# Kernel optimization log

Measured on AMD Instinct MI355X. Metric: run time of the kernel, lower is better.

The kernel has to match this reference:

```python
import jax, jax.numpy as jnp
import numpy as np

N, CIN, COUT, T, V, K = 32, 256, 256, 128, 25, 3
BN_EPS = 1e-5


def setup_inputs() -> dict:
    key = jax.random.key(0)
    k0, k1, k2 = jax.random.split(key, 3)
    x = jax.random.normal(k0, (N, CIN, T, V), dtype=jnp.float32)
    A = jax.random.normal(k1, (K, V, V), dtype=jnp.float32)
    W = jax.random.normal(k2, (K * COUT, CIN), dtype=jnp.float32) * 0.02
    b = jnp.zeros((K * COUT,), dtype=jnp.float32)
    gamma = jnp.ones((COUT,), dtype=jnp.float32)
    beta = jnp.zeros((COUT,), dtype=jnp.float32)
    return {"x": x, "A": A, "W": W, "b": b, "gamma": gamma, "beta": beta}


def reference(x, A, W, b, gamma, beta):
    n, c, t, v = x.shape
    k = A.shape[0]
    # 1x1 conv (conv_pos='pre'): [n,c,t,v] x [k*cout, c] -> [n, k*cout, t, v]
    y = jnp.einsum('nctv,oc->notv', x, W) + b[None, :, None, None]
    # split subsets and contract joints against the k adjacency matrices
    y = y.reshape(n, k, -1, t, v)
    y = jnp.einsum('nkctv,kvw->nctw', y, A)
    # BatchNorm2d (training-mode batch stats over n,t,v per channel)
    mu = jnp.mean(y, axis=(0, 2, 3), keepdims=True)
    var = jnp.var(y, axis=(0, 2, 3), keepdims=True)
    yn = (y - mu) * jax.lax.rsqrt(var + BN_EPS)
    out = gamma[None, :, None, None] * yn + beta[None, :, None, None]
    # with_res=False -> residual is 0; ReLU activation
    return jax.nn.relu(out)
```

## Files before the change

### kernel.cpp

```cpp
#include <hip/hip_runtime.h>
#include <cstddef>

#define NN   32
#define CIN  256
#define COUT 256
#define TT   128
#define VV   25
#define KK   3
#define TV   (TT*VV)
#define NTVC (NN*TT*VV)
#define BN_EPS 1e-5f

#define YT_LD 104
#define XS_LD 264

typedef __attribute__((ext_vector_type(8))) short bf16x8;
typedef __attribute__((ext_vector_type(4))) float f32x4;

__device__ __forceinline__ unsigned short f2bf(float f) {
    unsigned int u = __float_as_uint(f);
    u = (u + 0x7fffu + ((u >> 16) & 1u)) >> 16;
    return (unsigned short)u;
}

__device__ __forceinline__ uint2 pk4(f32x4 v) {
    uint2 r;
    asm("v_cvt_pk_bf16_f32 %0, %1, %2" : "=v"(r.x) : "v"(v[0]), "v"(v[1]));
    asm("v_cvt_pk_bf16_f32 %0, %1, %2" : "=v"(r.y) : "v"(v[2]), "v"(v[3]));
    return r;
}

__global__ __launch_bounds__(256)
void convert_w_kernel(const float* __restrict__ W, unsigned short* __restrict__ Wb) {
    int i = blockIdx.x * 256 + threadIdx.x;
    Wb[i] = f2bf(W[i]);
}

__global__ __launch_bounds__(256)
void transpose_x_kernel(const float* __restrict__ x, unsigned short* __restrict__ xT) {
    __shared__ float T[64][65];
    const int n   = blockIdx.z;
    const int s0  = blockIdx.x * 64;
    const int c0  = blockIdx.y * 64;
    const int tid = threadIdx.x;
    const int r    = tid >> 4;
    const int col4 = (tid & 15) * 4;

    const float* xp = x + (size_t)(n * CIN + c0) * TV + s0;
    for (int rr = r; rr < 64; rr += 16) {
        float4 v = *(const float4*)(xp + (size_t)rr * TV + col4);
        T[rr][col4 + 0] = v.x; T[rr][col4 + 1] = v.y;
        T[rr][col4 + 2] = v.z; T[rr][col4 + 3] = v.w;
    }
    __syncthreads();
    unsigned short* op = xT + ((size_t)n * TV + s0) * CIN + c0;
    for (int ss = r; ss < 64; ss += 16) {
        ushort4 o;
        o.x = f2bf(T[col4 + 0][ss]);
        o.y = f2bf(T[col4 + 1][ss]);
        o.z = f2bf(T[col4 + 2][ss]);
        o.w = f2bf(T[col4 + 3][ss]);
        *(ushort4*)(op + (size_t)ss * CIN + col4) = o;
    }
}

__global__ __launch_bounds__(1024)
void gemm_adj_kernel(const unsigned short* __restrict__ xT,
                     const unsigned short* __restrict__ Wb,
                     const float* __restrict__ A,
                     const float* __restrict__ b,
                     float* __restrict__ y2,
                     float* __restrict__ statsN)
{
    __shared__ __align__(16) unsigned short U[CIN * YT_LD];
    __shared__ __align__(16) unsigned short Ab[32 * 96];

    const int tid  = threadIdx.x;
    const int lane = tid & 63;
    const int wg   = tid >> 6;
    const int ln15 = lane & 15;
    const int quad = lane >> 4;
    const int tp   = blockIdx.x & 63;
    const int n    = blockIdx.x >> 6;
    const int t0   = tp * 2;

    {
        const unsigned short* xsrc = xT + ((size_t)n * TV + (size_t)t0 * VV) * CIN;
        for (int ch = tid; ch < 1600; ch += 1024) {
            const int s = ch >> 5, c8 = ch & 31;
            *(bf16x8*)&U[s * XS_LD + c8 * 8] = *(const bf16x8*)&xsrc[ch * 8];
        }
        const bf16x8 z = {0,0,0,0,0,0,0,0};
        for (int ch = tid; ch < 231; ch += 1024) {
            const int rr = 50 + ch / 33, c8 = ch - (ch / 33) * 33;
            *(bf16x8*)&U[rr * XS_LD + c8 * 8] = z;
        }
        for (int i = tid; i < 32 * 96; i += 1024) {
            const int w = i / 96, kv = i - w * 96;
            const int k = kv >> 5, v = kv & 31;
            Ab[i] = f2bf((v < VV && w < VV) ? A[k * VV * VV + v * VV + w] : 0.f);
        }
    }

    f32x4 acc[4][3];
    #pragma unroll
    for (int nt = 0; nt < 3; ++nt) {
        const float bv = b[48 * wg + 16 * nt + ln15];
        #pragma unroll
        for (int mt = 0; mt < 4; ++mt)
            #pragma unroll
            for (int r = 0; r < 4; ++r)
                acc[mt][nt][r] = bv;
    }

    __syncthreads();

    const int soff[4] = {0, 16, 25, 41};
    const unsigned short* wp = Wb + (size_t)(48 * wg + ln15) * CIN + quad * 8;
    bf16x8 wbuf[2][3];
    #pragma unroll
    for (int nt = 0; nt < 3; ++nt)
        wbuf[0][nt] = *(const bf16x8*)(wp + (size_t)nt * 16 * CIN);

    #pragma unroll
    for (int ks = 0; ks < 8; ++ks) {
        const int cur = ks & 1, nxt = cur ^ 1;
        if (ks < 7) {
            #pragma unroll
            for (int nt = 0; nt < 3; ++nt)
                wbuf[nxt][nt] = *(const bf16x8*)(wp + (size_t)nt * 16 * CIN + (ks + 1) * 32);
        }
        bf16x8 xfr[4];
        #pragma unroll
        for (int mt = 0; mt < 4; ++mt)
            xfr[mt] = *(const bf16x8*)&U[(soff[mt] + ln15) * XS_LD + ks * 32 + quad * 8];
        #pragma unroll
        for (int mt = 0; mt < 4; ++mt)
            #pragma unroll
            for (int nt = 0; nt < 3; ++nt)
                acc[mt][nt] = __builtin_amdgcn_mfma_f32_16x16x32_bf16(
                                  xfr[mt], wbuf[cur][nt], acc[mt][nt], 0, 0, 0);
    }

    __syncthreads();

    for (int i = tid; i < CIN * 21; i += 1024) {
        const int c = i / 21, rr = i - c * 21;
        const int k = rr / 7, v = VV + (rr - k * 7);
        U[c * YT_LD + k * 32 + v] = 0;
    }

    const int obase = 48 * wg + ln15;

    auto write_half = [&](int h) {
        const int mtF = 2 * h, mtP = 2 * h + 1;
        {
            const int v0 = quad * 4;
            #pragma unroll
            for (int nt = 0; nt < 3; ++nt) {
                const int o = obase + 16 * nt;
                *(uint2*)&U[(o & 255) * YT_LD + (o >> 8) * 32 + v0] = pk4(acc[mtF][nt]);
            }
        }
        if (quad < 2) {
            const int v0 = 16 + quad * 4;
            #pragma unroll
            for (int nt = 0; nt < 3; ++nt) {
                const int o = obase + 16 * nt;
                *(uint2*)&U[(o & 255) * YT_LD + (o >> 8) * 32 + v0] = pk4(acc[mtP][nt]);
            }
        } else if (quad == 2) {
            #pragma unroll
            for (int nt = 0; nt < 3; ++nt) {
                const int o = obase + 16 * nt;
                U[(o & 255) * YT_LD + (o >> 8) * 32 + 24] = f2bf(acc[mtP][nt][0]);
            }
        }
    };

    bf16x8 bq[3][2];
    float bsum1[4], bsum2[4];
    #pragma unroll
    for (int r = 0; r < 4; ++r) { bsum1[r] = 0.f; bsum2[r] = 0.f; }
    const int cb = wg * 16;

    #pragma unroll
    for (int h = 0; h < 2; ++h) {
        if (h) __syncthreads();
        write_half(h);
        __syncthreads();

        if (h == 0) {
            #pragma unroll
            for (int k = 0; k < 3; ++k)
                #pragma unroll
                for (int nw = 0; nw < 2; ++nw)
                    bq[k][nw] = *(const bf16x8*)&Ab[(16 * nw + ln15) * 96 + k * 32 + quad * 8];
        }

        f32x4 a2[2];
        #pragma unroll
        for (int nw = 0; nw < 2; ++nw)
            #pragma unroll
            for (int r = 0; r < 4; ++r) a2[nw][r] = 0.f;
        #pragma unroll
        for (int k = 0; k < 3; ++k) {
            const bf16x8 af = *(const bf16x8*)&U[(cb + ln15) * YT_LD + k * 32 + quad * 8];
            a2[0] = __builtin_amdgcn_mfma_f32_16x16x32_bf16(af, bq[k][0], a2[0], 0, 0, 0);
            a2[1] = __builtin_amdgcn_mfma_f32_16x16x32_bf16(af, bq[k][1], a2[1], 0, 0, 0);
        }
        const int t = t0 + h;
        float* op = y2 + (size_t)n * COUT * TV
                       + (size_t)(cb + 4 * quad) * TV + (size_t)t * VV;
        #pragma unroll
        for (int r = 0; r < 4; ++r) {
            const float va = a2[0][r];
            const float vb = a2[1][r];
            op[r * TV + ln15] = va;
            if (ln15 < 9) op[r * TV + 16 + ln15] = vb;
            const float vbm = (ln15 < 9) ? vb : 0.f;
            bsum1[r] += va + vbm;
            bsum2[r] += va * va + vbm * vbm;
        }
    }

    #pragma unroll
    for (int r = 0; r < 4; ++r) {
        float s1 = bsum1[r], s2 = bsum2[r];
        #pragma unroll
        for (int off = 1; off < 16; off <<= 1) {
            s1 += __shfl_xor(s1, off);
            s2 += __shfl_xor(s2, off);
        }
        if (ln15 == 0) {
            const int c = cb + 4 * quad + r;
            atomicAdd(&statsN[n * 512 + c], s1);
            atomicAdd(&statsN[n * 512 + 256 + c], s2);
        }
    }
}

__global__ void bn_stats_kernel(const float* __restrict__ statsN,
                                const float* __restrict__ gamma,
                                const float* __restrict__ beta,
                                float* __restrict__ ss)
{
    int c = threadIdx.x;
    float s1 = 0.f, s2 = 0.f;
    for (int g = 0; g < NN; ++g) {
        s1 += statsN[g * 512 + c];
        s2 += statsN[g * 512 + 256 + c];
    }
    float mu  = s1 * (1.f / NTVC);
    float var = s2 * (1.f / NTVC) - mu * mu;
    float sc  = gamma[c] * rsqrtf(var + BN_EPS);
    ss[c]        = sc;
    ss[COUT + c] = beta[c] - mu * sc;
}

__global__ __launch_bounds__(256)
void bn_apply_kernel(float* __restrict__ y, const float* __restrict__ ss)
{
    int i = blockIdx.x * 256 + threadIdx.x;
    int f = i * 4;
    int cch = (f / TV) & (COUT - 1);
    float sc = ss[cch], sh = ss[COUT + cch];
    float4 v = ((float4*)y)[i];
    v.x = fmaxf(v.x * sc + sh, 0.f);
    v.y = fmaxf(v.y * sc + sh, 0.f);
    v.z = fmaxf(v.z * sc + sh, 0.f);
    v.w = fmaxf(v.w * sc + sh, 0.f);
    ((float4*)y)[i] = v;
}

extern "C" void kernel_launch(void* const* d_in, const int* in_sizes, int n_in,
                              void* d_out, int out_size, void* d_ws, size_t ws_size,
                              hipStream_t stream)
{
    const float* x     = (const float*)d_in[0];
    const float* A     = (const float*)d_in[1];
    const float* W     = (const float*)d_in[2];
    const float* b     = (const float*)d_in[3];
    const float* gamma = (const float*)d_in[4];
    const float* beta  = (const float*)d_in[5];
    float* out = (float*)d_out;

    float* statsN = (float*)d_ws;
    float* ss     = (float*)((char*)d_ws + 65536);
    unsigned short* Wb  = (unsigned short*)((char*)d_ws + 67584);
    unsigned short* xTb = (unsigned short*)((char*)d_ws + 67584 + (size_t)KK * COUT * CIN * 2);

    hipMemsetAsync(statsN, 0, (size_t)NN * 512 * sizeof(float), stream);

    convert_w_kernel<<<(KK * COUT * CIN) / 256, 256, 0, stream>>>(W, Wb);
    transpose_x_kernel<<<dim3(TV / 64, CIN / 64, NN), 256, 0, stream>>>(x, xTb);
    gemm_adj_kernel<<<NN * (TT / 2), 1024, 0, stream>>>(xTb, Wb, A, b, out, statsN);
    bn_stats_kernel<<<1, 256, 0, stream>>>(statsN, gamma, beta, ss);
    bn_apply_kernel<<<(NN * COUT * TT * VV) / (4 * 256), 256, 0, stream>>>(out, ss);
}
```

Baseline: 386.1 us.

## Process one timestep per 512-thread block with more N-tiles per wave

The fused GEMM+adjacency kernel now handles one timestep per block with 8 waves instead of two timesteps with 16 waves. Each wave covers 96 output channels over two M-tiles, looping over two weight column groups. The two-half write/adjacency phase collapses into a single pass. The launch bounds ask for 4 blocks per CU. The aim is better occupancy and fewer barriers, at the cost of reloading weights from global memory for half as many rows per block and doubling the number of atomics.

```diff
diff --git a/kernel.cpp b/kernel.cpp
--- a/kernel.cpp
+++ b/kernel.cpp
@@ -64,7 +64,7 @@
     }
 }
 
-__global__ __launch_bounds__(1024)
+__global__ __launch_bounds__(512, 4)
 void gemm_adj_kernel(const unsigned short* __restrict__ xT,
                      const unsigned short* __restrict__ Wb,
                      const float* __restrict__ A,
@@ -80,34 +80,33 @@
     const int wg   = tid >> 6;
     const int ln15 = lane & 15;
     const int quad = lane >> 4;
-    const int tp   = blockIdx.x & 63;
-    const int n    = blockIdx.x >> 6;
-    const int t0   = tp * 2;
+    const int t    = blockIdx.x & 127;
+    const int n    = blockIdx.x >> 7;
 
     {
-        const unsigned short* xsrc = xT + ((size_t)n * TV + (size_t)t0 * VV) * CIN;
-        for (int ch = tid; ch < 1600; ch += 1024) {
+        const unsigned short* xsrc = xT + ((size_t)n * TV + (size_t)t * VV) * CIN;
+        for (int ch = tid; ch < 800; ch += 512) {
             const int s = ch >> 5, c8 = ch & 31;
             *(bf16x8*)&U[s * XS_LD + c8 * 8] = *(const bf16x8*)&xsrc[ch * 8];
         }
         const bf16x8 z = {0,0,0,0,0,0,0,0};
-        for (int ch = tid; ch < 231; ch += 1024) {
-            const int rr = 50 + ch / 33, c8 = ch - (ch / 33) * 33;
+        for (int ch = tid; ch < 231; ch += 512) {
+            const int rr = 25 + ch / 33, c8 = ch - (ch / 33) * 33;
             *(bf16x8*)&U[rr * XS_LD + c8 * 8] = z;
         }
-        for (int i = tid; i < 32 * 96; i += 1024) {
+        for (int i = tid; i < 32 * 96; i += 512) {
             const int w = i / 96, kv = i - w * 96;
             const int k = kv >> 5, v = kv & 31;
             Ab[i] = f2bf((v < VV && w < VV) ? A[k * VV * VV + v * VV + w] : 0.f);
         }
     }
 
-    f32x4 acc[4][3];
-    #pragma unroll
-    for (int nt = 0; nt < 3; ++nt) {
-        const float bv = b[48 * wg + 16 * nt + ln15];
-        #pragma unroll
-        for (int mt = 0; mt < 4; ++mt)
+    f32x4 acc[2][6];
+    #pragma unroll
+    for (int nt = 0; nt < 6; ++nt) {
+        const float bv = b[96 * wg + 16 * nt + ln15];
+        #pragma unroll
+        for (int mt = 0; mt < 2; ++mt)
             #pragma unroll
             for (int r = 0; r < 4; ++r)
                 acc[mt][nt][r] = bv;
@@ -115,89 +114,81 @@
 
     __syncthreads();
 
-    const int soff[4] = {0, 16, 25, 41};
-    const unsigned short* wp = Wb + (size_t)(48 * wg + ln15) * CIN + quad * 8;
-    bf16x8 wbuf[2][3];
-    #pragma unroll
-    for (int nt = 0; nt < 3; ++nt)
-        wbuf[0][nt] = *(const bf16x8*)(wp + (size_t)nt * 16 * CIN);
-
-    #pragma unroll
-    for (int ks = 0; ks < 8; ++ks) {
-        const int cur = ks & 1, nxt = cur ^ 1;
-        if (ks < 7) {
-            #pragma unroll
-            for (int nt = 0; nt < 3; ++nt)
-                wbuf[nxt][nt] = *(const bf16x8*)(wp + (size_t)nt * 16 * CIN + (ks + 1) * 32);
-        }
-        bf16x8 xfr[4];
-        #pragma unroll
-        for (int mt = 0; mt < 4; ++mt)
-            xfr[mt] = *(const bf16x8*)&U[(soff[mt] + ln15) * XS_LD + ks * 32 + quad * 8];
-        #pragma unroll
-        for (int mt = 0; mt < 4; ++mt)
-            #pragma unroll
-            for (int nt = 0; nt < 3; ++nt)
-                acc[mt][nt] = __builtin_amdgcn_mfma_f32_16x16x32_bf16(
-                                  xfr[mt], wbuf[cur][nt], acc[mt][nt], 0, 0, 0);
-    }
-
-    __syncthreads();
-
-    for (int i = tid; i < CIN * 21; i += 1024) {
+    #pragma unroll
+    for (int kp = 0; kp < 2; ++kp) {
+        const unsigned short* wp = Wb + (size_t)(96 * wg + 48 * kp + ln15) * CIN + quad * 8;
+        bf16x8 wbuf[2][3];
+        #pragma unroll
+        for (int nt = 0; nt < 3; ++nt)
+            wbuf[0][nt] = *(const bf16x8*)(wp + (size_t)nt * 16 * CIN);
+
+        #pragma unroll
+        for (int ks = 0; ks < 8; ++ks) {
+            const int cur = ks & 1, nxt = cur ^ 1;
+            if (ks < 7) {
+                #pragma unroll
+                for (int nt = 0; nt < 3; ++nt)
+                    wbuf[nxt][nt] = *(const bf16x8*)(wp + (size_t)nt * 16 * CIN + (ks + 1) * 32);
+            }
+            bf16x8 xfr[2];
+            #pragma unroll
+            for (int mt = 0; mt < 2; ++mt)
+                xfr[mt] = *(const bf16x8*)&U[(16 * mt + ln15) * XS_LD + ks * 32 + quad * 8];
+            #pragma unroll
+            for (int mt = 0; mt < 2; ++mt)
+                #pragma unroll
+                for (int nt = 0; nt < 3; ++nt)
+                    acc[mt][3 * kp + nt] = __builtin_amdgcn_mfma_f32_16x16x32_bf16(
+                                      xfr[mt], wbuf[cur][nt], acc[mt][3 * kp + nt], 0, 0, 0);
+        }
+    }
+
+    __syncthreads();
+
+    for (int i = tid; i < CIN * 21; i += 512) {
         const int c = i / 21, rr = i - c * 21;
         const int k = rr / 7, v = VV + (rr - k * 7);
         U[c * YT_LD + k * 32 + v] = 0;
     }
 
-    const int obase = 48 * wg + ln15;
-
-    auto write_half = [&](int h) {
-        const int mtF = 2 * h, mtP = 2 * h + 1;
+    {
+        const int obase = 96 * wg + ln15;
         {
             const int v0 = quad * 4;
             #pragma unroll
-            for (int nt = 0; nt < 3; ++nt) {
+            for (int nt = 0; nt < 6; ++nt) {
                 const int o = obase + 16 * nt;
-                *(uint2*)&U[(o & 255) * YT_LD + (o >> 8) * 32 + v0] = pk4(acc[mtF][nt]);
+                *(uint2*)&U[(o & 255) * YT_LD + (o >> 8) * 32 + v0] = pk4(acc[0][nt]);
             }
         }
         if (quad < 2) {
             const int v0 = 16 + quad * 4;
             #pragma unroll
-            for (int nt = 0; nt < 3; ++nt) {
+            for (int nt = 0; nt < 6; ++nt) {
                 const int o = obase + 16 * nt;
-                *(uint2*)&U[(o & 255) * YT_LD + (o >> 8) * 32 + v0] = pk4(acc[mtP][nt]);
+                *(uint2*)&U[(o & 255) * YT_LD + (o >> 8) * 32 + v0] = pk4(acc[1][nt]);
             }
         } else if (quad == 2) {
             #pragma unroll
-            for (int nt = 0; nt < 3; ++nt) {
+            for (int nt = 0; nt < 6; ++nt) {
                 const int o = obase + 16 * nt;
-                U[(o & 255) * YT_LD + (o >> 8) * 32 + 24] = f2bf(acc[mtP][nt][0]);
-            }
-        }
-    };
+                U[(o & 255) * YT_LD + (o >> 8) * 32 + 24] = f2bf(acc[1][nt][0]);
+            }
+        }
+    }
+
+    __syncthreads();
 
     bf16x8 bq[3][2];
-    float bsum1[4], bsum2[4];
-    #pragma unroll
-    for (int r = 0; r < 4; ++r) { bsum1[r] = 0.f; bsum2[r] = 0.f; }
-    const int cb = wg * 16;
-
-    #pragma unroll
-    for (int h = 0; h < 2; ++h) {
-        if (h) __syncthreads();
-        write_half(h);
-        __syncthreads();
-
-        if (h == 0) {
-            #pragma unroll
-            for (int k = 0; k < 3; ++k)
-                #pragma unroll
-                for (int nw = 0; nw < 2; ++nw)
-                    bq[k][nw] = *(const bf16x8*)&Ab[(16 * nw + ln15) * 96 + k * 32 + quad * 8];
-        }
-
+    #pragma unroll
+    for (int k = 0; k < 3; ++k)
+        #pragma unroll
+        for (int nw = 0; nw < 2; ++nw)
+            bq[k][nw] = *(const bf16x8*)&Ab[(16 * nw + ln15) * 96 + k * 32 + quad * 8];
+
+    #pragma unroll
+    for (int cbi = 0; cbi < 2; ++cbi) {
+        const int cb = wg * 32 + cbi * 16;
         f32x4 a2[2];
         #pragma unroll
         for (int nw = 0; nw < 2; ++nw)
@@ -209,9 +200,9 @@
             a2[0] = __builtin_amdgcn_mfma_f32_16x16x32_bf16(af, bq[k][0], a2[0], 0, 0, 0);
             a2[1] = __builtin_amdgcn_mfma_f32_16x16x32_bf16(af, bq[k][1], a2[1], 0, 0, 0);
         }
-        const int t = t0 + h;
         float* op = y2 + (size_t)n * COUT * TV
                        + (size_t)(cb + 4 * quad) * TV + (size_t)t * VV;
+        float bsum1[4], bsum2[4];
         #pragma unroll
         for (int r = 0; r < 4; ++r) {
             const float va = a2[0][r];
@@ -219,23 +210,22 @@
             op[r * TV + ln15] = va;
             if (ln15 < 9) op[r * TV + 16 + ln15] = vb;
             const float vbm = (ln15 < 9) ? vb : 0.f;
-            bsum1[r] += va + vbm;
-            bsum2[r] += va * va + vbm * vbm;
-        }
-    }
-
-    #pragma unroll
-    for (int r = 0; r < 4; ++r) {
-        float s1 = bsum1[r], s2 = bsum2[r];
-        #pragma unroll
-        for (int off = 1; off < 16; off <<= 1) {
-            s1 += __shfl_xor(s1, off);
-            s2 += __shfl_xor(s2, off);
-        }
-        if (ln15 == 0) {
-            const int c = cb + 4 * quad + r;
-            atomicAdd(&statsN[n * 512 + c], s1);
-            atomicAdd(&statsN[n * 512 + 256 + c], s2);
+            bsum1[r] = va + vbm;
+            bsum2[r] = va * va + vbm * vbm;
+        }
+        #pragma unroll
+        for (int r = 0; r < 4; ++r) {
+            float s1 = bsum1[r], s2 = bsum2[r];
+            #pragma unroll
+            for (int off = 1; off < 16; off <<= 1) {
+                s1 += __shfl_xor(s1, off);
+                s2 += __shfl_xor(s2, off);
+            }
+            if (ln15 == 0) {
+                const int c = cb + 4 * quad + r;
+                atomicAdd(&statsN[n * 512 + c], s1);
+                atomicAdd(&statsN[n * 512 + 256 + c], s2);
+            }
         }
     }
 }
@@ -294,7 +284,7 @@
 
     convert_w_kernel<<<(KK * COUT * CIN) / 256, 256, 0, stream>>>(W, Wb);
     transpose_x_kernel<<<dim3(TV / 64, CIN / 64, NN), 256, 0, stream>>>(x, xTb);
-    gemm_adj_kernel<<<NN * (TT / 2), 1024, 0, stream>>>(xTb, Wb, A, b, out, statsN);
+    gemm_adj_kernel<<<NN * TT, 512, 0, stream>>>(xTb, Wb, A, b, out, statsN);
     bn_stats_kernel<<<1, 256, 0, stream>>>(statsN, gamma, beta, ss);
     bn_apply_kernel<<<(NN * COUT * TT * VV) / (4 * 256), 256, 0, stream>>>(out, ss);
 }
```

Result: slower. 475.0 us (+23.0%).
